# Performance work log

Hardware: AMD Instinct MI355X
Metric: run time of the kernel (lower is better)

The kernel has to match this reference:

```python
import jax, jax.numpy as jnp
import numpy as np

N_TYPES = 4
AEV_DIM = 384
HIDDEN = [160, 128, 96]
CELU_ALPHA = 0.1


def _init_params(key):
    dims = [AEV_DIM] + HIDDEN + [1]
    params = {}
    for li in range(len(dims) - 1):
        key, kw = jax.random.split(key)
        scale = 1.0 / np.sqrt(dims[li])
        # stacked over the N_TYPES per-atom-type experts
        params[f"W{li}"] = (jax.random.normal(kw, (N_TYPES, dims[li], dims[li + 1]), dtype=jnp.float32) * scale)
        params[f"b{li}"] = jnp.zeros((N_TYPES, dims[li + 1]), dtype=jnp.float32)
    return params


def setup_inputs() -> dict:
    key = jax.random.key(0)
    k1, k2, k3 = jax.random.split(key, 3)
    B, A = 2048, 64
    species = jax.random.randint(k1, (B, A), 0, N_TYPES, dtype=jnp.int64)
    aev = jax.random.normal(k2, (B, A, AEV_DIM), dtype=jnp.float32)
    inp = {"species": species, "aev": aev}
    inp.update(_init_params(k3))
    return inp


def _mlp(x, t, W0, b0, W1, b1, W2, b2, W3, b3):
    # x: [N, aev_dim] -> [N] per-atom energy for atom type t
    h = jax.nn.celu(x @ W0[t] + b0[t], alpha=CELU_ALPHA)
    h = jax.nn.celu(h @ W1[t] + b1[t], alpha=CELU_ALPHA)
    h = jax.nn.celu(h @ W2[t] + b2[t], alpha=CELU_ALPHA)
    return (h @ W3[t] + b3[t]).reshape(-1)


def reference(species, aev, W0, b0, W1, b1, W2, b2, W3, b3):
    B, A = species.shape
    sp = species.reshape(-1)            # [B*A]
    x = aev.reshape(-1, aev.shape[-1])  # [B*A, aev_dim]
    out = jnp.zeros(sp.shape, dtype=aev.dtype)  # padding_fill = 0
    for t in range(N_TYPES):  # fixed small expert set
        y = _mlp(x, t, W0, b0, W1, b1, W2, b2, W3, b3)
        out = jnp.where(sp == t, y, out)
    energies = out.reshape(B, A).sum(axis=1)  # reduce over atoms
    return species, energies
```

## Files before the change

kernel.cpp:

```cpp
#include <hip/hip_runtime.h>
#include <math.h>


#define NATOMS   131072
#define NMOL     2048
#define AEV      384
#define NTYPES   4
#define MBLK     64
#define PADTOT   (NATOMS + NTYPES * MBLK)
#define NBLK_MLP (PADTOT / MBLK)
#define NBLK_H   512

#define WB_L1 61440
#define WB_L2 81920
#define WB_T  94208

typedef __attribute__((ext_vector_type(8))) short bf16x8;
typedef __attribute__((ext_vector_type(4))) float f32x4;

__device__ __forceinline__ float celu01(float v) {
  return (v > 0.f) ? v : 0.1f * (expf(v * 10.f) - 1.f);
}
__device__ __forceinline__ unsigned short f2bf(float x) {
  unsigned u = __float_as_uint(x);
  return (unsigned short)((u + 0x7FFFu + ((u >> 16) & 1u)) >> 16);
}
__device__ __forceinline__ float bf2f(unsigned short h) {
  return __uint_as_float(((unsigned)h) << 16);
}


__global__ void k_init(const int* __restrict__ species, float* __restrict__ out,
                       int* __restrict__ perm) {
  const int i = blockIdx.x * 256 + threadIdx.x;
  perm[i] = -1;
  if (i < NATOMS) out[i] = (float)species[i];
  if (i < NMOL) out[NATOMS + i] = 0.f;
}

__global__ void k_hist(const int* __restrict__ species, int* __restrict__ hist) {
  const int tid = threadIdx.x, blk = blockIdx.x;
  const int sp = species[blk * 256 + tid];
  const int wv = tid >> 6;
  __shared__ int wc[4 * NTYPES];
#pragma unroll
  for (int t = 0; t < NTYPES; ++t) {
    const unsigned long long m = __ballot(sp == t);
    if ((tid & 63) == 0) wc[wv * NTYPES + t] = __popcll(m);
  }
  __syncthreads();
  if (tid < NTYPES)
    hist[tid * NBLK_H + blk] = wc[tid] + wc[4 + tid] + wc[8 + tid] + wc[12 + tid];
}

__global__ void k_scan(const int* __restrict__ hist, int* __restrict__ poff,
                       int* __restrict__ boff) {
  __shared__ int tot[NTYPES], base[NTYPES];
  const int tid = threadIdx.x, wv = tid >> 6, lane = tid & 63;
  int s = 0;
  for (int c = 0; c < 8; ++c) s += hist[wv * NBLK_H + c * 64 + lane];
  for (int off = 32; off; off >>= 1) s += __shfl_down(s, off);
  if (lane == 0) tot[wv] = s;
  __syncthreads();
  if (tid == 0) {
    int acc = 0; poff[0] = 0;
    for (int t = 0; t < NTYPES; ++t) {
      base[t] = acc;
      acc += ((tot[t] + 63) >> 6) << 6;
      poff[t + 1] = acc;
    }
  }
  __syncthreads();
  int carry = base[wv];
  for (int c = 0; c < 8; ++c) {
    const int orig = hist[wv * NBLK_H + c * 64 + lane];
    int v = orig;
    for (int off = 1; off < 64; off <<= 1) {
      const int u = __shfl_up(v, off);
      if (lane >= off) v += u;
    }
    boff[wv * NBLK_H + c * 64 + lane] = carry + v - orig;
    carry += __shfl(v, 63);
  }
}

__global__ void k_scatter(const int* __restrict__ species, const int* __restrict__ boff,
                          int* __restrict__ perm) {
  const int tid = threadIdx.x, blk = blockIdx.x;
  const int i = blk * 256 + tid;
  const int sp = species[i];
  const int wv = tid >> 6;
  __shared__ int wc[4 * NTYPES];
  unsigned long long msel = 0;
#pragma unroll
  for (int t = 0; t < NTYPES; ++t) {
    const unsigned long long m = __ballot(sp == t);
    if ((tid & 63) == 0) wc[wv * NTYPES + t] = __popcll(m);
    if (sp == t) msel = m;
  }
  __syncthreads();
  int woff = 0;
  for (int w = 0; w < wv; ++w) woff += wc[w * NTYPES + sp];
  const int rk = __builtin_amdgcn_mbcnt_hi((unsigned)(msel >> 32),
                 __builtin_amdgcn_mbcnt_lo((unsigned)msel, 0));
  perm[boff[sp * NBLK_H + blk] + woff + rk] = i;
}


__global__ void k_wprep(const float* __restrict__ W0, const float* __restrict__ W1,
                        const float* __restrict__ W2, unsigned short* __restrict__ WB) {
  const int t = blockIdx.y;
  const int f = blockIdx.x * 256 + threadIdx.x;
  int base, NT, N;
  const float* W;
  if (f < WB_L1)      { base = 0;     NT = 10; N = 160; W = W0 + (size_t)t * AEV * 160; }
  else if (f < WB_L2) { base = WB_L1; NT = 8;  N = 128; W = W1 + (size_t)t * 160 * 128; }
  else                { base = WB_L2; NT = 6;  N = 96;  W = W2 + (size_t)t * 128 * 96; }
  const int e = f - base, frag = e >> 9, r = e & 511, lane = r >> 3, j = r & 7;
  const int kt = frag / NT, nt = frag - kt * NT;
  const int k = kt * 32 + ((lane >> 4) << 3) + j, n = nt * 16 + (lane & 15);
  WB[(size_t)t * WB_T + f] = f2bf(W[k * N + n]);
}


__global__ __launch_bounds__(256, 3) void k_mlp(
    const float* __restrict__ aev, const unsigned short* __restrict__ WB,
    const float* __restrict__ b0, const float* __restrict__ b1,
    const float* __restrict__ b2, const float* __restrict__ b3,
    const float* __restrict__ W3,
    const int* __restrict__ poff, const int* __restrict__ perm,
    float* __restrict__ outE)
{
  __shared__ __align__(16) unsigned short LDSA[64 * 200];
  __shared__ __align__(16) unsigned short LDSB[64 * 168];
  __shared__ float red[256];
  __shared__ int   permS[64];

  const int tid  = threadIdx.x;
  const int lane = tid & 63;
  const int wv   = __builtin_amdgcn_readfirstlane(tid >> 6);
  const int quad = lane >> 4, l15 = lane & 15;
  const int slot0 = blockIdx.x * MBLK;

  if (tid < 64) permS[tid] = perm[slot0 + tid];
  int t_ = (slot0 >= poff[1]) + (slot0 >= poff[2]) + (slot0 >= poff[3]);
  if (t_ > 3) t_ = 3;
  const int t = __builtin_amdgcn_readfirstlane(t_);
  __syncthreads();

  const bf16x8* wb0 = (const bf16x8*)(WB + (size_t)t * WB_T);
  const bf16x8* wb1 = (const bf16x8*)(WB + (size_t)t * WB_T + WB_L1);
  const bf16x8* wb2 = (const bf16x8*)(WB + (size_t)t * WB_T + WB_L2);

  f32x4 acc0[10];
#pragma unroll
  for (int nt = 0; nt < 10; ++nt) {
    const float b = b0[t * 160 + nt * 16 + l15];
    acc0[nt] = (f32x4){b, b, b, b};
  }
  const int sm = tid >> 2, scg = tid & 3;
  const int sai = permS[sm];
  for (int h = 0; h < 2; ++h) {
    const float4* src = (const float4*)(aev + (size_t)(sai < 0 ? 0 : sai) * AEV + h * 192);
#pragma unroll 4
    for (int i = 0; i < 12; ++i) {
      const int c4 = scg + i * 4;
      float4 v = make_float4(0.f, 0.f, 0.f, 0.f);
      if (sai >= 0) v = src[c4];
      ushort4 p = {f2bf(v.x), f2bf(v.y), f2bf(v.z), f2bf(v.w)};
      *(ushort4*)&LDSA[sm * 200 + c4 * 4] = p;
    }
    __syncthreads();
    const int arow = (wv * 16 + l15) * 200 + quad * 8;
    for (int ks = 0; ks < 6; ++ks) {
      const bf16x8 a = *(const bf16x8*)&LDSA[arow + ks * 32];
      const int ksg = h * 6 + ks;
#pragma unroll
      for (int nt = 0; nt < 10; ++nt)
        acc0[nt] = __builtin_amdgcn_mfma_f32_16x16x32_bf16(a, wb0[(ksg * 10 + nt) * 64 + lane], acc0[nt], 0, 0, 0);
    }
    __syncthreads();
  }
  {
    const int hrow0 = wv * 16 + quad * 4;
#pragma unroll
    for (int nt = 0; nt < 10; ++nt)
#pragma unroll
      for (int r = 0; r < 4; ++r)
        LDSB[(hrow0 + r) * 168 + nt * 16 + l15] = f2bf(celu01(acc0[nt][r]));
  }
  __syncthreads();

  f32x4 acc1[8];
#pragma unroll
  for (int nt = 0; nt < 8; ++nt) {
    const float b = b1[t * 128 + nt * 16 + l15];
    acc1[nt] = (f32x4){b, b, b, b};
  }
  {
    const int arow = (wv * 16 + l15) * 168 + quad * 8;
    for (int ks = 0; ks < 5; ++ks) {
      const bf16x8 a = *(const bf16x8*)&LDSB[arow + ks * 32];
#pragma unroll
      for (int nt = 0; nt < 8; ++nt)
        acc1[nt] = __builtin_amdgcn_mfma_f32_16x16x32_bf16(a, wb1[(ks * 8 + nt) * 64 + lane], acc1[nt], 0, 0, 0);
    }
  }
  __syncthreads();
  {
    const int hrow0 = wv * 16 + quad * 4;
#pragma unroll
    for (int nt = 0; nt < 8; ++nt)
#pragma unroll
      for (int r = 0; r < 4; ++r)
        LDSA[(hrow0 + r) * 136 + nt * 16 + l15] = f2bf(celu01(acc1[nt][r]));
  }
  __syncthreads();

  f32x4 acc2[6];
#pragma unroll
  for (int nt = 0; nt < 6; ++nt) {
    const float b = b2[t * 96 + nt * 16 + l15];
    acc2[nt] = (f32x4){b, b, b, b};
  }
  {
    const int arow = (wv * 16 + l15) * 136 + quad * 8;
    for (int ks = 0; ks < 4; ++ks) {
      const bf16x8 a = *(const bf16x8*)&LDSA[arow + ks * 32];
#pragma unroll
      for (int nt = 0; nt < 6; ++nt)
        acc2[nt] = __builtin_amdgcn_mfma_f32_16x16x32_bf16(a, wb2[(ks * 6 + nt) * 64 + lane], acc2[nt], 0, 0, 0);
    }
  }
  __syncthreads();
  {
    const int hrow0 = wv * 16 + quad * 4;
#pragma unroll
    for (int nt = 0; nt < 6; ++nt)
#pragma unroll
      for (int r = 0; r < 4; ++r)
        LDSB[(hrow0 + r) * 104 + nt * 16 + l15] = f2bf(celu01(acc2[nt][r]));
  }
  __syncthreads();

  const float* w3 = W3 + t * 96;
  float part = 0.f;
#pragma unroll
  for (int q = 0; q < 24; ++q) {
    const int c = wv * 24 + q;
    part = fmaf(bf2f(LDSB[lane * 104 + c]), w3[c], part);
  }
  red[wv * 64 + lane] = part;
  __syncthreads();
  if (wv == 0) {
    const float e = red[lane] + red[64 + lane] + red[128 + lane] + red[192 + lane] + b3[t];
    const int ai = permS[lane];
    if (ai >= 0) atomicAdd(&outE[ai >> 6], e);
  }
}


extern "C" void kernel_launch(void* const* d_in, const int* in_sizes, int n_in,
                              void* d_out, int out_size, void* d_ws, size_t ws_size,
                              hipStream_t stream)
{
  const int*   species = (const int*)d_in[0];
  const float* aev     = (const float*)d_in[1];
  const float* W0 = (const float*)d_in[2];
  const float* b0 = (const float*)d_in[3];
  const float* W1 = (const float*)d_in[4];
  const float* b1 = (const float*)d_in[5];
  const float* W2 = (const float*)d_in[6];
  const float* b2 = (const float*)d_in[7];
  const float* W3 = (const float*)d_in[8];
  const float* b3 = (const float*)d_in[9];
  float* out = (float*)d_out;

  int* poff = (int*)d_ws;
  int* hist = poff + 8;
  int* boff = hist + NTYPES * NBLK_H;
  int* perm = boff + NTYPES * NBLK_H;
  unsigned short* WB = (unsigned short*)(perm + PADTOT);

  k_wprep  <<<dim3(WB_T / 256, NTYPES), 256, 0, stream>>>(W0, W1, W2, WB);
  k_init   <<<PADTOT / 256, 256, 0, stream>>>(species, out, perm);
  k_hist   <<<NBLK_H, 256, 0, stream>>>(species, hist);
  k_scan   <<<1, 256, 0, stream>>>(hist, poff, boff);
  k_scatter<<<NBLK_H, 256, 0, stream>>>(species, boff, perm);
  k_mlp    <<<NBLK_MLP, 256, 0, stream>>>(aev, WB, b0, b1, b2, b3, W3,
                                          poff, perm, out + NATOMS);
}
```

Baseline: 386.4 us.

## Fuse prep kernels, share one LDS arena, raise MLP occupancy, use fast exp

Merges the weight-prep, init and histogram kernels into one launch, which removes two kernel launches. In the MLP kernel, the two LDS buffers become a single arena and the first layer stages the AEV in four chunks of 96 instead of two of 192. This cuts LDS per block so more blocks can be resident, and the launch bound moves from 3 to 6 blocks per CU. It also unrolls the k loops and switches CELU to __expf, which may squeeze registers and add spills, and the extra chunk adds more barriers.

```diff
diff --git a/kernel.cpp b/kernel.cpp
--- a/kernel.cpp
+++ b/kernel.cpp
@@ -19,7 +19,7 @@
 typedef __attribute__((ext_vector_type(4))) float f32x4;
 
 __device__ __forceinline__ float celu01(float v) {
-  return (v > 0.f) ? v : 0.1f * (expf(v * 10.f) - 1.f);
+  return (v > 0.f) ? v : 0.1f * (__expf(v * 10.f) - 1.f);
 }
 __device__ __forceinline__ unsigned short f2bf(float x) {
   unsigned u = __float_as_uint(x);
@@ -30,28 +30,44 @@
 }
 
 
-__global__ void k_init(const int* __restrict__ species, float* __restrict__ out,
-                       int* __restrict__ perm) {
-  const int i = blockIdx.x * 256 + threadIdx.x;
+__global__ void k_pre(const int* __restrict__ species, float* __restrict__ out,
+                      int* __restrict__ perm, int* __restrict__ hist,
+                      const float* __restrict__ W0, const float* __restrict__ W1,
+                      const float* __restrict__ W2, unsigned short* __restrict__ WB) {
+  const int tid = threadIdx.x, blk = blockIdx.x;
+  const int i = blk * 256 + tid;
   perm[i] = -1;
   if (i < NATOMS) out[i] = (float)species[i];
   if (i < NMOL) out[NATOMS + i] = 0.f;
-}
-
-__global__ void k_hist(const int* __restrict__ species, int* __restrict__ hist) {
-  const int tid = threadIdx.x, blk = blockIdx.x;
-  const int sp = species[blk * 256 + tid];
-  const int wv = tid >> 6;
-  __shared__ int wc[4 * NTYPES];
-#pragma unroll
-  for (int t = 0; t < NTYPES; ++t) {
-    const unsigned long long m = __ballot(sp == t);
-    if ((tid & 63) == 0) wc[wv * NTYPES + t] = __popcll(m);
-  }
-  __syncthreads();
-  if (tid < NTYPES)
-    hist[tid * NBLK_H + blk] = wc[tid] + wc[4 + tid] + wc[8 + tid] + wc[12 + tid];
-}
+
+  for (int f = i; f < NTYPES * WB_T; f += PADTOT) {
+    const int t = f / WB_T, e0 = f - t * WB_T;
+    int base, NT, N;
+    const float* W;
+    if (e0 < WB_L1)      { base = 0;     NT = 10; N = 160; W = W0 + (size_t)t * AEV * 160; }
+    else if (e0 < WB_L2) { base = WB_L1; NT = 8;  N = 128; W = W1 + (size_t)t * 160 * 128; }
+    else                 { base = WB_L2; NT = 6;  N = 96;  W = W2 + (size_t)t * 128 * 96; }
+    const int e = e0 - base, frag = e >> 9, r = e & 511, lane = r >> 3, j = r & 7;
+    const int kt = frag / NT, nt = frag - kt * NT;
+    const int k = kt * 32 + ((lane >> 4) << 3) + j, n = nt * 16 + (lane & 15);
+    WB[(size_t)t * WB_T + e0] = f2bf(W[k * N + n]);
+  }
+
+  if (blk < NBLK_H) {
+    const int sp = species[i];
+    const int wv = tid >> 6;
+    __shared__ int wc[4 * NTYPES];
+#pragma unroll
+    for (int t = 0; t < NTYPES; ++t) {
+      const unsigned long long m = __ballot(sp == t);
+      if ((tid & 63) == 0) wc[wv * NTYPES + t] = __popcll(m);
+    }
+    __syncthreads();
+    if (tid < NTYPES)
+      hist[tid * NBLK_H + blk] = wc[tid] + wc[4 + tid] + wc[8 + tid] + wc[12 + tid];
+  }
+}
+
 
 __global__ void k_scan(const int* __restrict__ hist, int* __restrict__ poff,
                        int* __restrict__ boff) {
@@ -107,23 +123,7 @@
 }
 
 
-__global__ void k_wprep(const float* __restrict__ W0, const float* __restrict__ W1,
-                        const float* __restrict__ W2, unsigned short* __restrict__ WB) {
-  const int t = blockIdx.y;
-  const int f = blockIdx.x * 256 + threadIdx.x;
-  int base, NT, N;
-  const float* W;
-  if (f < WB_L1)      { base = 0;     NT = 10; N = 160; W = W0 + (size_t)t * AEV * 160; }
-  else if (f < WB_L2) { base = WB_L1; NT = 8;  N = 128; W = W1 + (size_t)t * 160 * 128; }
-  else                { base = WB_L2; NT = 6;  N = 96;  W = W2 + (size_t)t * 128 * 96; }
-  const int e = f - base, frag = e >> 9, r = e & 511, lane = r >> 3, j = r & 7;
-  const int kt = frag / NT, nt = frag - kt * NT;
-  const int k = kt * 32 + ((lane >> 4) << 3) + j, n = nt * 16 + (lane & 15);
-  WB[(size_t)t * WB_T + f] = f2bf(W[k * N + n]);
-}
-
-
-__global__ __launch_bounds__(256, 3) void k_mlp(
+__global__ __launch_bounds__(256, 6) void k_mlp(
     const float* __restrict__ aev, const unsigned short* __restrict__ WB,
     const float* __restrict__ b0, const float* __restrict__ b1,
     const float* __restrict__ b2, const float* __restrict__ b3,
@@ -131,8 +131,7 @@
     const int* __restrict__ poff, const int* __restrict__ perm,
     float* __restrict__ outE)
 {
-  __shared__ __align__(16) unsigned short LDSA[64 * 200];
-  __shared__ __align__(16) unsigned short LDSB[64 * 168];
+  __shared__ __align__(16) unsigned short ARENA[64 * 168];
   __shared__ float red[256];
   __shared__ int   permS[64];
 
@@ -160,21 +159,22 @@
   }
   const int sm = tid >> 2, scg = tid & 3;
   const int sai = permS[sm];
-  for (int h = 0; h < 2; ++h) {
-    const float4* src = (const float4*)(aev + (size_t)(sai < 0 ? 0 : sai) * AEV + h * 192);
-#pragma unroll 4
-    for (int i = 0; i < 12; ++i) {
-      const int c4 = scg + i * 4;
+  const float4* src = (const float4*)(aev + (size_t)(sai < 0 ? 0 : sai) * AEV);
+  for (int s = 0; s < 4; ++s) {
+#pragma unroll
+    for (int ii = 0; ii < 6; ++ii) {
+      const int c4 = scg + ii * 4;
       float4 v = make_float4(0.f, 0.f, 0.f, 0.f);
-      if (sai >= 0) v = src[c4];
+      if (sai >= 0) v = src[s * 24 + c4];
       ushort4 p = {f2bf(v.x), f2bf(v.y), f2bf(v.z), f2bf(v.w)};
-      *(ushort4*)&LDSA[sm * 200 + c4 * 4] = p;
+      *(ushort4*)&ARENA[sm * 104 + c4 * 4] = p;
     }
     __syncthreads();
-    const int arow = (wv * 16 + l15) * 200 + quad * 8;
-    for (int ks = 0; ks < 6; ++ks) {
-      const bf16x8 a = *(const bf16x8*)&LDSA[arow + ks * 32];
-      const int ksg = h * 6 + ks;
+    const int arow = (wv * 16 + l15) * 104 + quad * 8;
+#pragma unroll
+    for (int ks = 0; ks < 3; ++ks) {
+      const bf16x8 a = *(const bf16x8*)&ARENA[arow + ks * 32];
+      const int ksg = s * 3 + ks;
 #pragma unroll
       for (int nt = 0; nt < 10; ++nt)
         acc0[nt] = __builtin_amdgcn_mfma_f32_16x16x32_bf16(a, wb0[(ksg * 10 + nt) * 64 + lane], acc0[nt], 0, 0, 0);
@@ -187,7 +187,7 @@
     for (int nt = 0; nt < 10; ++nt)
 #pragma unroll
       for (int r = 0; r < 4; ++r)
-        LDSB[(hrow0 + r) * 168 + nt * 16 + l15] = f2bf(celu01(acc0[nt][r]));
+        ARENA[(hrow0 + r) * 168 + nt * 16 + l15] = f2bf(celu01(acc0[nt][r]));
   }
   __syncthreads();
 
@@ -199,8 +199,9 @@
   }
   {
     const int arow = (wv * 16 + l15) * 168 + quad * 8;
+#pragma unroll
     for (int ks = 0; ks < 5; ++ks) {
-      const bf16x8 a = *(const bf16x8*)&LDSB[arow + ks * 32];
+      const bf16x8 a = *(const bf16x8*)&ARENA[arow + ks * 32];
 #pragma unroll
       for (int nt = 0; nt < 8; ++nt)
         acc1[nt] = __builtin_amdgcn_mfma_f32_16x16x32_bf16(a, wb1[(ks * 8 + nt) * 64 + lane], acc1[nt], 0, 0, 0);
@@ -213,7 +214,7 @@
     for (int nt = 0; nt < 8; ++nt)
 #pragma unroll
       for (int r = 0; r < 4; ++r)
-        LDSA[(hrow0 + r) * 136 + nt * 16 + l15] = f2bf(celu01(acc1[nt][r]));
+        ARENA[(hrow0 + r) * 136 + nt * 16 + l15] = f2bf(celu01(acc1[nt][r]));
   }
   __syncthreads();
 
@@ -225,8 +226,9 @@
   }
   {
     const int arow = (wv * 16 + l15) * 136 + quad * 8;
+#pragma unroll
     for (int ks = 0; ks < 4; ++ks) {
-      const bf16x8 a = *(const bf16x8*)&LDSA[arow + ks * 32];
+      const bf16x8 a = *(const bf16x8*)&ARENA[arow + ks * 32];
 #pragma unroll
       for (int nt = 0; nt < 6; ++nt)
         acc2[nt] = __builtin_amdgcn_mfma_f32_16x16x32_bf16(a, wb2[(ks * 6 + nt) * 64 + lane], acc2[nt], 0, 0, 0);
@@ -239,7 +241,7 @@
     for (int nt = 0; nt < 6; ++nt)
 #pragma unroll
       for (int r = 0; r < 4; ++r)
-        LDSB[(hrow0 + r) * 104 + nt * 16 + l15] = f2bf(celu01(acc2[nt][r]));
+        ARENA[(hrow0 + r) * 104 + nt * 16 + l15] = f2bf(celu01(acc2[nt][r]));
   }
   __syncthreads();
 
@@ -248,7 +250,7 @@
 #pragma unroll
   for (int q = 0; q < 24; ++q) {
     const int c = wv * 24 + q;
-    part = fmaf(bf2f(LDSB[lane * 104 + c]), w3[c], part);
+    part = fmaf(bf2f(ARENA[lane * 104 + c]), w3[c], part);
   }
   red[wv * 64 + lane] = part;
   __syncthreads();
@@ -282,9 +284,7 @@
   int* perm = boff + NTYPES * NBLK_H;
   unsigned short* WB = (unsigned short*)(perm + PADTOT);
 
-  k_wprep  <<<dim3(WB_T / 256, NTYPES), 256, 0, stream>>>(W0, W1, W2, WB);
-  k_init   <<<PADTOT / 256, 256, 0, stream>>>(species, out, perm);
-  k_hist   <<<NBLK_H, 256, 0, stream>>>(species, hist);
+  k_pre    <<<PADTOT / 256, 256, 0, stream>>>(species, out, perm, hist, W0, W1, W2, WB);
   k_scan   <<<1, 256, 0, stream>>>(hist, poff, boff);
   k_scatter<<<NBLK_H, 256, 0, stream>>>(species, boff, perm);
   k_mlp    <<<NBLK_MLP, 256, 0, stream>>>(aev, WB, b0, b1, b2, b3, W3,
```

Result: no change. 384.0 us (-0.6%).
